# Kernel tuning notes

Hardware: AMD Instinct MI355X
Metric: run time of the kernel (lower is better)

Reference implementation:

```python
import jax, jax.numpy as jnp
import numpy as np

N = 50000
E = 800000
F = 64
HID = 64
HEADS = 4
NTYPES = 3


def layer_norm(x, g, b, eps=1e-5):
    mu = x.mean(-1, keepdims=True)
    var = ((x - mu) ** 2).mean(-1, keepdims=True)
    return (x - mu) * jax.lax.rsqrt(var + eps) * g + b


def gat_conv(x, src, dst, n, W, att_src, att_dst, bias, concat):
    # PyG GATConv: per-head linear transform, additive attention, segment softmax over dst.
    H, C = att_src.shape
    xp = (x @ W).reshape(n, H, C)                       # [N,H,C]
    a_s = (xp * att_src).sum(-1)                         # [N,H]
    a_d = (xp * att_dst).sum(-1)                         # [N,H]
    e = jax.nn.leaky_relu(a_s[src] + a_d[dst], 0.2)      # [Etot,H]
    m = jax.ops.segment_max(e, dst, num_segments=n)      # stable softmax per target
    ex = jnp.exp(e - m[dst])
    denom = jax.ops.segment_sum(ex, dst, num_segments=n)
    alpha = ex / (denom[dst] + 1e-16)                    # [Etot,H]
    msg = xp[src] * alpha[:, :, None]                    # [Etot,H,C]
    out = jax.ops.segment_sum(msg, dst, num_segments=n)  # [N,H,C]
    out = out.reshape(n, H * C) if concat else out.mean(1)
    return out + bias


def setup_inputs() -> dict:
    key = jax.random.key(0)
    ks = jax.random.split(key, 12)
    f32 = jnp.float32
    return {
        'node_features': jax.random.normal(ks[0], (N, F), f32),
        'node_types': jax.random.randint(ks[1], (N,), 0, NTYPES),
        'edge_index': jax.random.randint(ks[2], (2, E), 0, N),
        'type_emb': jax.random.normal(ks[3], (NTYPES, HID), f32) * 0.02,
        'proj_W': jax.random.normal(ks[4], (F, HID), f32) / np.sqrt(F).astype(np.float32),
        'proj_b': jnp.zeros((HID,), f32),
        'W0': jax.random.normal(ks[5], (HID, HEADS * HID), f32) / np.sqrt(HID).astype(np.float32),
        'att_src0': jax.random.normal(ks[6], (HEADS, HID), f32) * 0.1,
        'att_dst0': jax.random.normal(ks[7], (HEADS, HID), f32) * 0.1,
        'bias0': jnp.zeros((HEADS * HID,), f32),
        'ln0_g': jnp.ones((HEADS * HID,), f32),
        'ln0_b': jnp.zeros((HEADS * HID,), f32),
        'W1': jax.random.normal(ks[8], (HEADS * HID, HEADS * HID), f32) / np.sqrt(HEADS * HID).astype(np.float32),
        'att_src1': jax.random.normal(ks[9], (HEADS, HID), f32) * 0.1,
        'att_dst1': jax.random.normal(ks[10], (HEADS, HID), f32) * 0.1,
        'bias1': jnp.zeros((HID,), f32),
        'ln1_g': jnp.ones((HID,), f32),
        'ln1_b': jnp.zeros((HID,), f32),
    }


def reference(node_features, node_types, edge_index, type_emb, proj_W, proj_b,
              W0, att_src0, att_dst0, bias0, ln0_g, ln0_b,
              W1, att_src1, att_dst1, bias1, ln1_g, ln1_b):
    n = node_features.shape[0]
    loop = jnp.arange(n)
    src = jnp.concatenate([edge_index[0], loop])  # add_self_loops=True (PyG default)
    dst = jnp.concatenate([edge_index[1], loop])
    # input projection + node-type embedding
    x = node_features @ proj_W + proj_b + type_emb[node_types]
    # layer 0: concat heads -> [N, HEADS*HID]
    h = gat_conv(x, src, dst, n, W0, att_src0, att_dst0, bias0, True)
    h = jax.nn.relu(layer_norm(h, ln0_g, ln0_b))  # dropout is identity in eval
    # layer 1: mean over heads -> [N, HID]; residual skipped (shape mismatch 256 vs 64)
    h2 = gat_conv(h, src, dst, n, W1, att_src1, att_dst1, bias1, False)
    h2 = jax.nn.relu(layer_norm(h2, ln1_g, ln1_b))
    return h2
```

## Files before the change

### kernel.cpp

```cpp
#include <hip/hip_runtime.h>
#include <hip/hip_bf16.h>
#include <hip/hip_fp16.h>

typedef unsigned short u16;
typedef unsigned int u32;
typedef short s16x8 __attribute__((ext_vector_type(8)));
typedef float f32x4 __attribute__((ext_vector_type(4)));

__device__ __forceinline__ float bf2f(u16 u) {
  return __uint_as_float(((u32)u) << 16);
}

__device__ __forceinline__ u16 f2b(float f) {
  __hip_bfloat16 h = __float2bfloat16(f);
  return *(u16*)&h;
}

__device__ __forceinline__ u32 packbf(float lo, float hi) {
  return (u32)f2b(lo) | ((u32)f2b(hi) << 16);
}

__device__ __forceinline__ bool sniff_bf16(const void* ones) {
  u32 w = *(const u32*)ones;
  return (w >> 16) == (w & 0xFFFFu);
}

__device__ __forceinline__ float ldf(const void* p, size_t i, bool bf) {
  return bf ? bf2f(((const u16*)p)[i]) : ((const float*)p)[i];
}

__device__ __forceinline__ float rdlane_f(float v, int e) {
  return __uint_as_float((u32)__builtin_amdgcn_readlane((int)__float_as_uint(v), e));
}

__global__ void fill_f32(float* __restrict__ p, float v, size_t n) {
  size_t i = (size_t)blockIdx.x * blockDim.x + threadIdx.x;
  if (i < n) p[i] = v;
}

__global__ __launch_bounds__(256) void deg_count_k(const int* __restrict__ ei, int E, int N,
                                                   int* __restrict__ deg) {
  int i = blockIdx.x * 256 + threadIdx.x;
  if (i >= E + N) return;
  int d = (i < E) ? ei[E + i] : (i - E);
  atomicAdd(deg + d, 1);
}

__global__ __launch_bounds__(256) void scan_local_k(const int* __restrict__ deg,
                                                    int* __restrict__ off,
                                                    int* __restrict__ bsum, int N) {
  __shared__ int ps[256];
  int t = threadIdx.x;
  int i = blockIdx.x * 256 + t;
  int v = (i < N) ? deg[i] : 0;
  ps[t] = v;
  __syncthreads();
#pragma unroll
  for (int o = 1; o < 256; o <<= 1) {
    int u = (t >= o) ? ps[t - o] : 0;
    __syncthreads();
    ps[t] += u;
    __syncthreads();
  }
  if (i < N) off[i] = ps[t] - v;
  if (t == 255) bsum[blockIdx.x] = ps[255];
}

__global__ __launch_bounds__(1024) void scan_bsum_k(int* __restrict__ bsum, int nb) {
  __shared__ int ps[1024];
  int t = threadIdx.x;
  int v = (t < nb) ? bsum[t] : 0;
  ps[t] = v;
  __syncthreads();
#pragma unroll
  for (int o = 1; o < 1024; o <<= 1) {
    int u = (t >= o) ? ps[t - o] : 0;
    __syncthreads();
    ps[t] += u;
    __syncthreads();
  }
  if (t < nb) bsum[t] = ps[t] - v;
}

__global__ __launch_bounds__(256) void scan_add_k(int* __restrict__ off,
                                                  const int* __restrict__ bsum,
                                                  int* __restrict__ cur, int N, int Etot) {
  int i = blockIdx.x * 256 + threadIdx.x;
  if (i == 0) off[N] = Etot;
  if (i >= N) return;
  int o = off[i] + bsum[i >> 8];
  off[i] = o;
  cur[i] = o;
}

__global__ __launch_bounds__(256) void scatter_k(const int* __restrict__ ei, int E, int N,
                                                 int* __restrict__ cur, int* __restrict__ csr) {
  int i = blockIdx.x * 256 + threadIdx.x;
  if (i >= E + N) return;
  int s, d;
  if (i < E) { s = ei[i]; d = ei[E + i]; } else { s = i - E; d = s; }
  int p = atomicAdd(cur + d, 1);
  csr[p] = s;
}

__global__ __launch_bounds__(256) void wpack_k(const void* __restrict__ W,
                                               const void* __restrict__ ones,
                                               u16* __restrict__ Wp, int K) {
  bool bf = sniff_bf16(ones);
  int i = blockIdx.x * 256 + threadIdx.x;
  if (i >= K * 256) return;
  int j = i & 7;
  int q = (i >> 3) & 3;
  int c = (i >> 5) & 255;
  int kc = i >> 13;
  int k = kc * 32 + q * 8 + j;
  Wp[i] = f2b(ldf(W, (size_t)k * 256 + c, bf));
}

__global__ __launch_bounds__(256) void wpack64_k(const void* __restrict__ W,
                                                 const void* __restrict__ ones,
                                                 u16* __restrict__ Wp) {
  bool bf = sniff_bf16(ones);
  int i = blockIdx.x * 256 + threadIdx.x;
  if (i >= 64 * 64) return;
  int j = i & 7;
  int q = (i >> 3) & 3;
  int c = (i >> 5) & 63;
  int kc = i >> 11;
  int k = kc * 32 + q * 8 + j;
  Wp[i] = f2b(ldf(W, (size_t)k * 64 + c, bf));
}

__global__ __launch_bounds__(256) void attvec_k(const void* __restrict__ W,
                                                const void* __restrict__ atts,
                                                const void* __restrict__ attd,
                                                const void* __restrict__ ones,
                                                float* __restrict__ va, float* __restrict__ vd) {
  bool bf = sniff_bf16(ones);
  int t = threadIdx.x;
  int h = t >> 6, k = t & 63;
  float s = 0.f, d = 0.f;
  for (int c = 0; c < 64; c++) {
    float w = ldf(W, (size_t)k * 256 + h * 64 + c, bf);
    s += w * ldf(atts, h * 64 + c, bf);
    d += w * ldf(attd, h * 64 + c, bf);
  }
  va[t] = s;
  vd[t] = d;
}

__global__ __launch_bounds__(256) void proj_k(
    const void* __restrict__ nf, const int* __restrict__ ntype,
    const u16* __restrict__ Wpp, const void* __restrict__ pbias,
    const void* __restrict__ temb, const float* __restrict__ va,
    const float* __restrict__ vd, const void* __restrict__ ones,
    u16* __restrict__ x, float* __restrict__ aS, float* __restrict__ aD, int N) {
  bool bf = sniff_bf16(ones);
  __shared__ u16 xs[16][64];
  int t = threadIdx.x;
  int wave = t >> 6, lane = t & 63;
  int r = lane & 15, q = lane >> 4;
  int row0 = blockIdx.x * 16;
  int arow = row0 + r;
  if (arow >= N) arow = N - 1;
  f32x4 xacc = {0.f, 0.f, 0.f, 0.f};
#pragma unroll
  for (int kc = 0; kc < 2; kc++) {
    s16x8 a;
    if (bf) {
      a = *(const s16x8*)((const u16*)nf + (size_t)arow * 64 + kc * 32 + q * 8);
    } else {
      const float* fp = (const float*)nf + (size_t)arow * 64 + kc * 32 + q * 8;
#pragma unroll
      for (int j = 0; j < 8; j++) a[j] = (short)f2b(fp[j]);
    }
    int c = wave * 16 + r;
    s16x8 b = *(const s16x8*)(Wpp + (((size_t)kc * 64 + c) * 4 + q) * 8);
    xacc = __builtin_amdgcn_mfma_f32_16x16x32_bf16(a, b, xacc, 0, 0, 0);
  }
#pragma unroll
  for (int rg = 0; rg < 4; rg++) {
    int row = row0 + q * 4 + rg;
    int rl = (row < N) ? row : N - 1;
    int col = wave * 16 + r;
    int ty = ntype[rl];
    float v = xacc[rg] + ldf(pbias, col, bf) + ldf(temb, ty * 64 + col, bf);
    u16 xb = f2b(v);
    xs[q * 4 + rg][col] = xb;
    if (row < N) x[(size_t)row * 64 + col] = xb;
  }
  __syncthreads();
  float vs[4], vdl[4];
#pragma unroll
  for (int h = 0; h < 4; h++) { vs[h] = va[h * 64 + lane]; vdl[h] = vd[h * 64 + lane]; }
#pragma unroll
  for (int rr = 0; rr < 4; rr++) {
    int row = row0 + wave * 4 + rr;
    float xv = bf2f(xs[wave * 4 + rr][lane]);
    float ps[4], pd[4];
#pragma unroll
    for (int h = 0; h < 4; h++) { ps[h] = xv * vs[h]; pd[h] = xv * vdl[h]; }
#pragma unroll
    for (int o = 32; o > 0; o >>= 1) {
#pragma unroll
      for (int h = 0; h < 4; h++) {
        ps[h] += __shfl_xor(ps[h], o, 64);
        pd[h] += __shfl_xor(pd[h], o, 64);
      }
    }
    if (lane == 0 && row < N) {
#pragma unroll
      for (int h = 0; h < 4; h++) {
        aS[(size_t)row * 4 + h] = ps[h];
        aD[(size_t)row * 4 + h] = pd[h];
      }
    }
  }
}

__global__ __launch_bounds__(256) void agg0_k(
    const int* __restrict__ off, const int* __restrict__ csr,
    const float* __restrict__ aS, const float* __restrict__ aD,
    const u16* __restrict__ x, u16* __restrict__ Ag, int N) {
  int n = blockIdx.x * 4 + (threadIdx.x >> 6);
  int lane = threadIdx.x & 63;
  if (n >= N) return;
  int start = off[n], end = off[n + 1];
  float4 ad4 = *(const float4*)(aD + (size_t)n * 4);
  float ad[4] = {ad4.x, ad4.y, ad4.z, ad4.w};
  float den[4] = {0.f, 0.f, 0.f, 0.f};
  float acc[4] = {0.f, 0.f, 0.f, 0.f};
  const u16* xl = x + lane;

  for (int cs = start; cs < end; cs += 64) {
    int cnt = end - cs; if (cnt > 64) cnt = 64;
    int s = 0;
    float ex[4] = {0.f, 0.f, 0.f, 0.f};
    if (lane < cnt) {
      s = csr[cs + lane];
      float4 as4 = *(const float4*)(aS + (size_t)s * 4);
      float av[4] = {as4.x, as4.y, as4.z, as4.w};
#pragma unroll
      for (int h = 0; h < 4; h++) {
        float v = av[h] + ad[h];
        v = (v > 0.f ? v : 0.2f * v) - 3.0f;
        ex[h] = __expf(v);
        den[h] += ex[h];
      }
    }
#pragma unroll 4
    for (int e = 0; e < cnt; e++) {
      int se = __builtin_amdgcn_readlane(s, e);
      float w0 = rdlane_f(ex[0], e);
      float w1 = rdlane_f(ex[1], e);
      float w2 = rdlane_f(ex[2], e);
      float w3 = rdlane_f(ex[3], e);
      float xv = bf2f(xl[(size_t)se * 64]);
      acc[0] += w0 * xv;
      acc[1] += w1 * xv;
      acc[2] += w2 * xv;
      acc[3] += w3 * xv;
    }
  }
#pragma unroll
  for (int h = 0; h < 4; h++) {
#pragma unroll
    for (int o = 32; o > 0; o >>= 1) den[h] += __shfl_xor(den[h], o, 64);
    acc[h] /= (den[h] + 1e-16f);
  }
#pragma unroll
  for (int h = 0; h < 4; h++) Ag[(size_t)n * 256 + h * 64 + lane] = f2b(acc[h]);
}

__global__ __launch_bounds__(256) void l0post_k(
    const u16* __restrict__ Ag, const u16* __restrict__ Wp,
    const void* __restrict__ bias, const void* __restrict__ g,
    const void* __restrict__ b, const void* __restrict__ ones,
    u16* __restrict__ hb, int N) {
  bool bf = sniff_bf16(ones);
  __shared__ float sm_s[4][16], sm_q[4][16];
  int t = threadIdx.x;
  int wave = t >> 6, lane = t & 63;
  int r = lane & 15, q = lane >> 4;
  int row0 = blockIdx.x * 16;
  int arow = row0 + r;
  if (arow >= N) arow = N - 1;
  const u16* ap = Ag + (size_t)arow * 256 + wave * 64 + q * 8;
  f32x4 acc[4] = {{0.f, 0.f, 0.f, 0.f}, {0.f, 0.f, 0.f, 0.f},
                  {0.f, 0.f, 0.f, 0.f}, {0.f, 0.f, 0.f, 0.f}};
#pragma unroll
  for (int kc = 0; kc < 2; kc++) {
    s16x8 a = *(const s16x8*)(ap + kc * 32);
#pragma unroll
    for (int ct = 0; ct < 4; ct++) {
      int c = wave * 64 + ct * 16 + r;
      s16x8 bb = *(const s16x8*)(Wp + (((size_t)kc * 256 + c) * 4 + q) * 8);
      acc[ct] = __builtin_amdgcn_mfma_f32_16x16x32_bf16(a, bb, acc[ct], 0, 0, 0);
    }
  }
  float yv[4][4];
  float s_p[4] = {0.f, 0.f, 0.f, 0.f};
  float q_p[4] = {0.f, 0.f, 0.f, 0.f};
#pragma unroll
  for (int ct = 0; ct < 4; ct++) {
    float bc = ldf(bias, wave * 64 + ct * 16 + r, bf);
#pragma unroll
    for (int rg = 0; rg < 4; rg++) {
      float y = acc[ct][rg] + bc;
      yv[ct][rg] = y;
      s_p[rg] += y;
      q_p[rg] += y * y;
    }
  }
#pragma unroll
  for (int o = 1; o < 16; o <<= 1) {
#pragma unroll
    for (int rg = 0; rg < 4; rg++) {
      s_p[rg] += __shfl_xor(s_p[rg], o, 64);
      q_p[rg] += __shfl_xor(q_p[rg], o, 64);
    }
  }
  if (r == 0) {
#pragma unroll
    for (int rg = 0; rg < 4; rg++) {
      sm_s[wave][q * 4 + rg] = s_p[rg];
      sm_q[wave][q * 4 + rg] = q_p[rg];
    }
  }
  __syncthreads();
#pragma unroll
  for (int rg = 0; rg < 4; rg++) {
    int lr = q * 4 + rg;
    int row = row0 + lr;
    float mu = (sm_s[0][lr] + sm_s[1][lr] + sm_s[2][lr] + sm_s[3][lr]) * (1.f / 256.f);
    float vq = (sm_q[0][lr] + sm_q[1][lr] + sm_q[2][lr] + sm_q[3][lr]) * (1.f / 256.f) - mu * mu;
    float inv = rsqrtf(vq + 1e-5f);
    if (row < N) {
#pragma unroll
      for (int ct = 0; ct < 4; ct++) {
        int c = wave * 64 + ct * 16 + r;
        float o_ = (yv[ct][rg] - mu) * inv * ldf(g, c, bf) + ldf(b, c, bf);
        hb[(size_t)row * 256 + c] = f2b(fmaxf(o_, 0.f));
      }
    }
  }
}

template <int K>
__global__ __launch_bounds__(256) void gemm_mfma_k(
    const u16* __restrict__ A, const u16* __restrict__ Wp,
    const void* __restrict__ atts, const void* __restrict__ attd,
    const void* __restrict__ ones,
    u16* __restrict__ C, float* __restrict__ aS, float* __restrict__ aD, int N) {
  bool bf = sniff_bf16(ones);
  int t = threadIdx.x;
  int wave = t >> 6, lane = t & 63;
  int r = lane & 15, q = lane >> 4;
  int row0 = blockIdx.x * 16;
  int colw = wave * 64;
  int arow = row0 + r;
  if (arow >= N) arow = N - 1;
  const u16* ap = A + (size_t)arow * K + q * 8;
  f32x4 acc[4] = {{0.f, 0.f, 0.f, 0.f}, {0.f, 0.f, 0.f, 0.f},
                  {0.f, 0.f, 0.f, 0.f}, {0.f, 0.f, 0.f, 0.f}};
#pragma unroll
  for (int kc = 0; kc < K / 32; kc++) {
    s16x8 a = *(const s16x8*)(ap + kc * 32);
#pragma unroll
    for (int ct = 0; ct < 4; ct++) {
      int c = colw + ct * 16 + r;
      s16x8 b = *(const s16x8*)(Wp + (((size_t)kc * 256 + c) * 4 + q) * 8);
      acc[ct] = __builtin_amdgcn_mfma_f32_16x16x32_bf16(a, b, acc[ct], 0, 0, 0);
    }
  }
#pragma unroll
  for (int ct = 0; ct < 4; ct++) {
#pragma unroll
    for (int rg = 0; rg < 4; rg++) {
      int row = row0 + q * 4 + rg;
      if (row < N) C[(size_t)row * 256 + colw + ct * 16 + r] = f2b(acc[ct][rg]);
    }
  }
  float sp[4] = {0.f, 0.f, 0.f, 0.f};
  float dp[4] = {0.f, 0.f, 0.f, 0.f};
#pragma unroll
  for (int ct = 0; ct < 4; ct++) {
    int c = colw + ct * 16 + r;
    float av = ldf(atts, c, bf);
    float dv = ldf(attd, c, bf);
#pragma unroll
    for (int rg = 0; rg < 4; rg++) {
      sp[rg] += acc[ct][rg] * av;
      dp[rg] += acc[ct][rg] * dv;
    }
  }
#pragma unroll
  for (int o = 1; o < 16; o <<= 1) {
#pragma unroll
    for (int rg = 0; rg < 4; rg++) {
      sp[rg] += __shfl_xor(sp[rg], o, 64);
      dp[rg] += __shfl_xor(dp[rg], o, 64);
    }
  }
  if (r == 0) {
#pragma unroll
    for (int rg = 0; rg < 4; rg++) {
      int row = row0 + q * 4 + rg;
      if (row < N) {
        aS[(size_t)row * 4 + wave] = sp[rg];
        aD[(size_t)row * 4 + wave] = dp[rg];
      }
    }
  }
}

__global__ __launch_bounds__(256) void agg1_k(
    const int* __restrict__ off, const int* __restrict__ csr,
    const float* __restrict__ aS, const float* __restrict__ aD,
    const u16* __restrict__ xp,
    const void* __restrict__ bias, const void* __restrict__ g,
    const void* __restrict__ b, void* __restrict__ out, int N) {
  bool bf = sniff_bf16(g);
  int n = blockIdx.x * 4 + (threadIdx.x >> 6);
  int lane = threadIdx.x & 63;
  if (n >= N) return;
  int start = off[n], end = off[n + 1];
  bool hiSel = (lane & 32) != 0;
  float4 ad4 = *(const float4*)(aD + (size_t)n * 4);
  float ad[4] = {ad4.x, ad4.y, ad4.z, ad4.w};
  float den[4] = {0.f, 0.f, 0.f, 0.f};
  float acc[4] = {0.f, 0.f, 0.f, 0.f};
  const u32* xp32 = (const u32*)xp;

  for (int cs = start; cs < end; cs += 64) {
    int cnt = end - cs; if (cnt > 64) cnt = 64;
    int s = 0;
    float ex[4] = {0.f, 0.f, 0.f, 0.f};
    if (lane < cnt) {
      s = csr[cs + lane];
      float4 as4 = *(const float4*)(aS + (size_t)s * 4);
      float av[4] = {as4.x, as4.y, as4.z, as4.w};
#pragma unroll
      for (int h = 0; h < 4; h++) {
        float v = av[h] + ad[h];
        v = (v > 0.f ? v : 0.2f * v) - 3.0f;
        ex[h] = __expf(v);
        den[h] += ex[h];
      }
    }
#pragma unroll 4
    for (int e = 0; e < cnt; e++) {
      int se = __builtin_amdgcn_readlane(s, e);
      float w0 = rdlane_f(ex[0], e);
      float w1 = rdlane_f(ex[1], e);
      float w2 = rdlane_f(ex[2], e);
      float w3 = rdlane_f(ex[3], e);
      float wA = hiSel ? w1 : w0;
      float wB = hiSel ? w3 : w2;
      const u32* xr = xp32 + (size_t)se * 128 + lane;
      u32 dA = xr[0];
      u32 dB = xr[64];
      acc[0] += wA * __uint_as_float(dA << 16);
      acc[1] += wA * __uint_as_float(dA & 0xffff0000u);
      acc[2] += wB * __uint_as_float(dB << 16);
      acc[3] += wB * __uint_as_float(dB & 0xffff0000u);
    }
  }
#pragma unroll
  for (int h = 0; h < 4; h++) {
#pragma unroll
    for (int o = 32; o > 0; o >>= 1) den[h] += __shfl_xor(den[h], o, 64);
  }
  {
    float dA = (hiSel ? den[1] : den[0]) + 1e-16f;
    float dB = (hiSel ? den[3] : den[2]) + 1e-16f;
    acc[0] /= dA; acc[1] /= dA;
    acc[2] /= dB; acc[3] /= dB;
  }
  float p0 = acc[0] + acc[2];
  float p1 = acc[1] + acc[3];
  p0 += __shfl_xor(p0, 32, 64);
  p1 += __shfl_xor(p1, 32, 64);
  int c = 2 * (lane & 31);
  float z0 = 0.25f * p0 + ldf(bias, c, bf);
  float z1 = 0.25f * p1 + ldf(bias, c + 1, bf);
  float sum = z0 + z1;
#pragma unroll
  for (int o = 32; o > 0; o >>= 1) sum += __shfl_xor(sum, o, 64);
  float mu = sum * (1.f / 128.f);
  float d0 = z0 - mu, d1 = z1 - mu;
  float sq = d0 * d0 + d1 * d1;
#pragma unroll
  for (int o = 32; o > 0; o >>= 1) sq += __shfl_xor(sq, o, 64);
  float inv = rsqrtf(sq * (1.f / 128.f) + 1e-5f);
  float y0 = fmaxf(d0 * inv * ldf(g, c, bf) + ldf(b, c, bf), 0.f);
  float y1 = fmaxf(d1 * inv * ldf(g, c + 1, bf) + ldf(b, c + 1, bf), 0.f);
  if (lane < 32) {
    if (bf) {
      ((u32*)out)[(size_t)n * 32 + lane] = packbf(y0, y1);
    } else {
      ((float2*)out)[(size_t)n * 32 + lane] = make_float2(y0, y1);
    }
  }
}

extern "C" void kernel_launch(void* const* d_in, const int* in_sizes, int n_in,
                              void* d_out, int out_size, void* d_ws, size_t ws_size,
                              hipStream_t stream) {
  const void* nf   = d_in[0];
  const int* ntyp  = (const int*)d_in[1];
  const int* ei    = (const int*)d_in[2];
  const void* temb = d_in[3];
  const void* pW   = d_in[4];
  const void* pb   = d_in[5];
  const void* W0   = d_in[6];
  const void* as0  = d_in[7];
  const void* ad0  = d_in[8];
  const void* b0   = d_in[9];
  const void* g0   = d_in[10];
  const void* be0  = d_in[11];
  const void* W1   = d_in[12];
  const void* as1  = d_in[13];
  const void* ad1  = d_in[14];
  const void* b1   = d_in[15];
  const void* g1   = d_in[16];
  const void* be1  = d_in[17];

  int N = in_sizes[0] / 64;
  int E = in_sizes[2] / 2;
  int Etot = E + N;

  u16* Wp0 = (u16*)d_ws;
  u16* Wp1 = Wp0 + 64 * 256;
  u16* Wpp = Wp1 + 256 * 256;
  u16* xb  = Wpp + 64 * 64;
  u16* Ag  = xb + (size_t)N * 64;
  u16* A   = Ag + (size_t)N * 256;
  u16* hb  = A + (size_t)N * 256;
  float* va = (float*)(hb + (size_t)N * 256);
  float* vd = va + 256;
  float* aS = vd + 256;
  float* aD = aS + (size_t)N * 4;
  int* deg  = (int*)(aD + (size_t)N * 4);
  int* off  = deg + N;
  int* csr  = off + N + 1;
  int* bsum = csr + Etot;

  dim3 b256(256);
  int nodeBlocks = (N + 3) / 4;
  int edgeBlocksT = (Etot + 255) / 256;
  int gemmBlocks = (N + 15) / 16;
  int scanBlocks = (N + 255) / 256;

  fill_f32<<<(N + 255) / 256, b256, 0, stream>>>((float*)deg, 0.f, (size_t)N);
  deg_count_k<<<edgeBlocksT, b256, 0, stream>>>(ei, E, N, deg);
  scan_local_k<<<scanBlocks, b256, 0, stream>>>(deg, off, bsum, N);
  scan_bsum_k<<<1, 1024, 0, stream>>>(bsum, scanBlocks);
  scan_add_k<<<scanBlocks, b256, 0, stream>>>(off, bsum, deg, N, Etot);
  scatter_k<<<edgeBlocksT, b256, 0, stream>>>(ei, E, N, deg, csr);
  wpack_k<<<(64 * 256 + 255) / 256, b256, 0, stream>>>(W0, g0, Wp0, 64);
  wpack_k<<<(256 * 256 + 255) / 256, b256, 0, stream>>>(W1, g0, Wp1, 256);
  wpack64_k<<<(64 * 64 + 255) / 256, b256, 0, stream>>>(pW, g0, Wpp);
  attvec_k<<<1, b256, 0, stream>>>(W0, as0, ad0, g0, va, vd);

  proj_k<<<gemmBlocks, b256, 0, stream>>>(nf, ntyp, Wpp, pb, temb, va, vd, g0,
                                          xb, aS, aD, N);
  agg0_k<<<nodeBlocks, b256, 0, stream>>>(off, csr, aS, aD, xb, Ag, N);
  l0post_k<<<gemmBlocks, b256, 0, stream>>>(Ag, Wp0, b0, g0, be0, g0, hb, N);

  gemm_mfma_k<256><<<gemmBlocks, b256, 0, stream>>>(hb, Wp1, as1, ad1, g0, A, aS, aD, N);
  agg1_k<<<nodeBlocks, b256, 0, stream>>>(off, csr, aS, aD, A, b1, g1, be1, d_out, N);
}
```

Measured before the change: 447.7 us.

## Fuse layer-0 post GEMM with layer-1 GEMM and fold attention scores into projection

Merges the layer-0 post-processing kernel (GEMM, bias, LayerNorm, ReLU) with the layer-1 GEMM, so the normalized hidden tile stays in shared memory instead of going out to and back from a global buffer. The attention score vectors are precomputed into a packed weight matrix plus per-type constants, letting the projection kernel produce aS/aD with one extra MFMA instead of a shared-memory pass and shuffle reductions. The aggregation loop unroll is also raised from 4 to 8. This cuts one N×256 round trip and a kernel launch, at the cost of more shared memory per block and some bf16 rounding of the folded attention weights.

```diff
diff --git a/kernel.cpp b/kernel.cpp
--- a/kernel.cpp
+++ b/kernel.cpp
@@ -131,32 +131,60 @@
   Wp[i] = f2b(ldf(W, (size_t)k * 64 + c, bf));
 }
 
-__global__ __launch_bounds__(256) void attvec_k(const void* __restrict__ W,
-                                                const void* __restrict__ atts,
-                                                const void* __restrict__ attd,
-                                                const void* __restrict__ ones,
-                                                float* __restrict__ va, float* __restrict__ vd) {
+__global__ __launch_bounds__(256) void attvec2_k(
+    const void* __restrict__ W0, const void* __restrict__ atts,
+    const void* __restrict__ attd, const void* __restrict__ pW,
+    const void* __restrict__ pb, const void* __restrict__ temb,
+    const void* __restrict__ ones, u16* __restrict__ Wpe, float* __restrict__ ca) {
   bool bf = sniff_bf16(ones);
+  __shared__ float va[256], vd[256];
   int t = threadIdx.x;
   int h = t >> 6, k = t & 63;
-  float s = 0.f, d = 0.f;
-  for (int c = 0; c < 64; c++) {
-    float w = ldf(W, (size_t)k * 256 + h * 64 + c, bf);
-    s += w * ldf(atts, h * 64 + c, bf);
-    d += w * ldf(attd, h * 64 + c, bf);
-  }
-  va[t] = s;
-  vd[t] = d;
-}
-
-__global__ __launch_bounds__(256) void proj_k(
+  {
+    float s = 0.f, d = 0.f;
+    for (int c = 0; c < 64; c++) {
+      float w = ldf(W0, (size_t)k * 256 + h * 64 + c, bf);
+      s += w * ldf(atts, h * 64 + c, bf);
+      d += w * ldf(attd, h * 64 + c, bf);
+    }
+    va[t] = s;
+    vd[t] = d;
+  }
+  __syncthreads();
+  {
+    int i = k;
+    float wa = 0.f, wd = 0.f;
+    for (int kk = 0; kk < 64; kk++) {
+      float wv = ldf(pW, (size_t)i * 64 + kk, bf);
+      wa += wv * va[h * 64 + kk];
+      wd += wv * vd[h * 64 + kk];
+    }
+    int kc = i >> 5, q = (i >> 3) & 3, j = i & 7;
+    Wpe[((kc * 16 + h) * 4 + q) * 8 + j] = f2b(wa);
+    Wpe[((kc * 16 + 4 + h) * 4 + q) * 8 + j] = f2b(wd);
+  }
+  Wpe[256 + t] = 0;
+  Wpe[768 + t] = 0;
+  if (t < 12) {
+    int ty = t >> 2, hh = t & 3;
+    float sa = 0.f, sd = 0.f;
+    for (int kk = 0; kk < 64; kk++) {
+      float bv = ldf(pb, kk, bf) + ldf(temb, ty * 64 + kk, bf);
+      sa += bv * va[hh * 64 + kk];
+      sd += bv * vd[hh * 64 + kk];
+    }
+    ca[t] = sa;
+    ca[12 + t] = sd;
+  }
+}
+
+__global__ __launch_bounds__(256) void proj2_k(
     const void* __restrict__ nf, const int* __restrict__ ntype,
-    const u16* __restrict__ Wpp, const void* __restrict__ pbias,
-    const void* __restrict__ temb, const float* __restrict__ va,
-    const float* __restrict__ vd, const void* __restrict__ ones,
+    const u16* __restrict__ Wpp, const u16* __restrict__ Wpe,
+    const void* __restrict__ pbias, const void* __restrict__ temb,
+    const float* __restrict__ ca, const void* __restrict__ ones,
     u16* __restrict__ x, float* __restrict__ aS, float* __restrict__ aD, int N) {
   bool bf = sniff_bf16(ones);
-  __shared__ u16 xs[16][64];
   int t = threadIdx.x;
   int wave = t >> 6, lane = t & 63;
   int r = lane & 15, q = lane >> 4;
@@ -164,6 +192,7 @@
   int arow = row0 + r;
   if (arow >= N) arow = N - 1;
   f32x4 xacc = {0.f, 0.f, 0.f, 0.f};
+  f32x4 eacc = {0.f, 0.f, 0.f, 0.f};
 #pragma unroll
   for (int kc = 0; kc < 2; kc++) {
     s16x8 a;
@@ -174,46 +203,27 @@
 #pragma unroll
       for (int j = 0; j < 8; j++) a[j] = (short)f2b(fp[j]);
     }
-    int c = wave * 16 + r;
-    s16x8 b = *(const s16x8*)(Wpp + (((size_t)kc * 64 + c) * 4 + q) * 8);
-    xacc = __builtin_amdgcn_mfma_f32_16x16x32_bf16(a, b, xacc, 0, 0, 0);
+    {
+      int c = wave * 16 + r;
+      s16x8 b = *(const s16x8*)(Wpp + (((size_t)kc * 64 + c) * 4 + q) * 8);
+      xacc = __builtin_amdgcn_mfma_f32_16x16x32_bf16(a, b, xacc, 0, 0, 0);
+    }
+    if (wave == 3) {
+      s16x8 b = *(const s16x8*)(Wpe + (((size_t)kc * 16 + r) * 4 + q) * 8);
+      eacc = __builtin_amdgcn_mfma_f32_16x16x32_bf16(a, b, eacc, 0, 0, 0);
+    }
   }
 #pragma unroll
   for (int rg = 0; rg < 4; rg++) {
     int row = row0 + q * 4 + rg;
-    int rl = (row < N) ? row : N - 1;
+    if (row >= N) continue;
     int col = wave * 16 + r;
-    int ty = ntype[rl];
+    int ty = ntype[row];
     float v = xacc[rg] + ldf(pbias, col, bf) + ldf(temb, ty * 64 + col, bf);
-    u16 xb = f2b(v);
-    xs[q * 4 + rg][col] = xb;
-    if (row < N) x[(size_t)row * 64 + col] = xb;
-  }
-  __syncthreads();
-  float vs[4], vdl[4];
-#pragma unroll
-  for (int h = 0; h < 4; h++) { vs[h] = va[h * 64 + lane]; vdl[h] = vd[h * 64 + lane]; }
-#pragma unroll
-  for (int rr = 0; rr < 4; rr++) {
-    int row = row0 + wave * 4 + rr;
-    float xv = bf2f(xs[wave * 4 + rr][lane]);
-    float ps[4], pd[4];
-#pragma unroll
-    for (int h = 0; h < 4; h++) { ps[h] = xv * vs[h]; pd[h] = xv * vdl[h]; }
-#pragma unroll
-    for (int o = 32; o > 0; o >>= 1) {
-#pragma unroll
-      for (int h = 0; h < 4; h++) {
-        ps[h] += __shfl_xor(ps[h], o, 64);
-        pd[h] += __shfl_xor(pd[h], o, 64);
-      }
-    }
-    if (lane == 0 && row < N) {
-#pragma unroll
-      for (int h = 0; h < 4; h++) {
-        aS[(size_t)row * 4 + h] = ps[h];
-        aD[(size_t)row * 4 + h] = pd[h];
-      }
+    x[(size_t)row * 64 + col] = f2b(v);
+    if (wave == 3 && r < 8) {
+      if (r < 4) aS[(size_t)row * 4 + r] = eacc[rg] + ca[ty * 4 + r];
+      else       aD[(size_t)row * 4 + (r - 4)] = eacc[rg] + ca[12 + ty * 4 + (r - 4)];
     }
   }
 }
@@ -248,7 +258,7 @@
         den[h] += ex[h];
       }
     }
-#pragma unroll 4
+#pragma unroll 8
     for (int e = 0; e < cnt; e++) {
       int se = __builtin_amdgcn_readlane(s, e);
       float w0 = rdlane_f(ex[0], e);
@@ -272,12 +282,15 @@
   for (int h = 0; h < 4; h++) Ag[(size_t)n * 256 + h * 64 + lane] = f2b(acc[h]);
 }
 
-__global__ __launch_bounds__(256) void l0post_k(
-    const u16* __restrict__ Ag, const u16* __restrict__ Wp,
-    const void* __restrict__ bias, const void* __restrict__ g,
-    const void* __restrict__ b, const void* __restrict__ ones,
-    u16* __restrict__ hb, int N) {
+__global__ __launch_bounds__(256) void l0g1_k(
+    const u16* __restrict__ Ag, const u16* __restrict__ Wp0,
+    const void* __restrict__ bias0, const void* __restrict__ g0,
+    const void* __restrict__ be0, const u16* __restrict__ Wp1,
+    const void* __restrict__ atts, const void* __restrict__ attd,
+    const void* __restrict__ ones,
+    u16* __restrict__ C, float* __restrict__ aS, float* __restrict__ aD, int N) {
   bool bf = sniff_bf16(ones);
+  __shared__ u16 hs[16][264];
   __shared__ float sm_s[4][16], sm_q[4][16];
   int t = threadIdx.x;
   int wave = t >> 6, lane = t & 63;
@@ -285,91 +298,75 @@
   int row0 = blockIdx.x * 16;
   int arow = row0 + r;
   if (arow >= N) arow = N - 1;
-  const u16* ap = Ag + (size_t)arow * 256 + wave * 64 + q * 8;
+  {
+    const u16* ap = Ag + (size_t)arow * 256 + wave * 64 + q * 8;
+    f32x4 acc[4] = {{0.f, 0.f, 0.f, 0.f}, {0.f, 0.f, 0.f, 0.f},
+                    {0.f, 0.f, 0.f, 0.f}, {0.f, 0.f, 0.f, 0.f}};
+#pragma unroll
+    for (int kc = 0; kc < 2; kc++) {
+      s16x8 a = *(const s16x8*)(ap + kc * 32);
+#pragma unroll
+      for (int ct = 0; ct < 4; ct++) {
+        int c = wave * 64 + ct * 16 + r;
+        s16x8 b = *(const s16x8*)(Wp0 + (((size_t)kc * 256 + c) * 4 + q) * 8);
+        acc[ct] = __builtin_amdgcn_mfma_f32_16x16x32_bf16(a, b, acc[ct], 0, 0, 0);
+      }
+    }
+    float yv[4][4];
+    float s_p[4] = {0.f, 0.f, 0.f, 0.f};
+    float q_p[4] = {0.f, 0.f, 0.f, 0.f};
+#pragma unroll
+    for (int ct = 0; ct < 4; ct++) {
+      float bc = ldf(bias0, wave * 64 + ct * 16 + r, bf);
+#pragma unroll
+      for (int rg = 0; rg < 4; rg++) {
+        float y = acc[ct][rg] + bc;
+        yv[ct][rg] = y;
+        s_p[rg] += y;
+        q_p[rg] += y * y;
+      }
+    }
+#pragma unroll
+    for (int o = 1; o < 16; o <<= 1) {
+#pragma unroll
+      for (int rg = 0; rg < 4; rg++) {
+        s_p[rg] += __shfl_xor(s_p[rg], o, 64);
+        q_p[rg] += __shfl_xor(q_p[rg], o, 64);
+      }
+    }
+    if (r == 0) {
+#pragma unroll
+      for (int rg = 0; rg < 4; rg++) {
+        sm_s[wave][q * 4 + rg] = s_p[rg];
+        sm_q[wave][q * 4 + rg] = q_p[rg];
+      }
+    }
+    __syncthreads();
+#pragma unroll
+    for (int rg = 0; rg < 4; rg++) {
+      int lr = q * 4 + rg;
+      float mu = (sm_s[0][lr] + sm_s[1][lr] + sm_s[2][lr] + sm_s[3][lr]) * (1.f / 256.f);
+      float vq = (sm_q[0][lr] + sm_q[1][lr] + sm_q[2][lr] + sm_q[3][lr]) * (1.f / 256.f) - mu * mu;
+      float inv = rsqrtf(vq + 1e-5f);
+#pragma unroll
+      for (int ct = 0; ct < 4; ct++) {
+        int c = wave * 64 + ct * 16 + r;
+        float o_ = (yv[ct][rg] - mu) * inv * ldf(g0, c, bf) + ldf(be0, c, bf);
+        hs[lr][c] = f2b(fmaxf(o_, 0.f));
+      }
+    }
+  }
+  __syncthreads();
+  int colw = wave * 64;
   f32x4 acc[4] = {{0.f, 0.f, 0.f, 0.f}, {0.f, 0.f, 0.f, 0.f},
                   {0.f, 0.f, 0.f, 0.f}, {0.f, 0.f, 0.f, 0.f}};
 #pragma unroll
-  for (int kc = 0; kc < 2; kc++) {
-    s16x8 a = *(const s16x8*)(ap + kc * 32);
-#pragma unroll
-    for (int ct = 0; ct < 4; ct++) {
-      int c = wave * 64 + ct * 16 + r;
-      s16x8 bb = *(const s16x8*)(Wp + (((size_t)kc * 256 + c) * 4 + q) * 8);
-      acc[ct] = __builtin_amdgcn_mfma_f32_16x16x32_bf16(a, bb, acc[ct], 0, 0, 0);
-    }
-  }
-  float yv[4][4];
-  float s_p[4] = {0.f, 0.f, 0.f, 0.f};
-  float q_p[4] = {0.f, 0.f, 0.f, 0.f};
-#pragma unroll
-  for (int ct = 0; ct < 4; ct++) {
-    float bc = ldf(bias, wave * 64 + ct * 16 + r, bf);
-#pragma unroll
-    for (int rg = 0; rg < 4; rg++) {
-      float y = acc[ct][rg] + bc;
-      yv[ct][rg] = y;
-      s_p[rg] += y;
-      q_p[rg] += y * y;
-    }
-  }
-#pragma unroll
-  for (int o = 1; o < 16; o <<= 1) {
-#pragma unroll
-    for (int rg = 0; rg < 4; rg++) {
-      s_p[rg] += __shfl_xor(s_p[rg], o, 64);
-      q_p[rg] += __shfl_xor(q_p[rg], o, 64);
-    }
-  }
-  if (r == 0) {
-#pragma unroll
-    for (int rg = 0; rg < 4; rg++) {
-      sm_s[wave][q * 4 + rg] = s_p[rg];
-      sm_q[wave][q * 4 + rg] = q_p[rg];
-    }
-  }
-  __syncthreads();
-#pragma unroll
-  for (int rg = 0; rg < 4; rg++) {
-    int lr = q * 4 + rg;
-    int row = row0 + lr;
-    float mu = (sm_s[0][lr] + sm_s[1][lr] + sm_s[2][lr] + sm_s[3][lr]) * (1.f / 256.f);
-    float vq = (sm_q[0][lr] + sm_q[1][lr] + sm_q[2][lr] + sm_q[3][lr]) * (1.f / 256.f) - mu * mu;
-    float inv = rsqrtf(vq + 1e-5f);
-    if (row < N) {
-#pragma unroll
-      for (int ct = 0; ct < 4; ct++) {
-        int c = wave * 64 + ct * 16 + r;
-        float o_ = (yv[ct][rg] - mu) * inv * ldf(g, c, bf) + ldf(b, c, bf);
-        hb[(size_t)row * 256 + c] = f2b(fmaxf(o_, 0.f));
-      }
-    }
-  }
-}
-
-template <int K>
-__global__ __launch_bounds__(256) void gemm_mfma_k(
-    const u16* __restrict__ A, const u16* __restrict__ Wp,
-    const void* __restrict__ atts, const void* __restrict__ attd,
-    const void* __restrict__ ones,
-    u16* __restrict__ C, float* __restrict__ aS, float* __restrict__ aD, int N) {
-  bool bf = sniff_bf16(ones);
-  int t = threadIdx.x;
-  int wave = t >> 6, lane = t & 63;
-  int r = lane & 15, q = lane >> 4;
-  int row0 = blockIdx.x * 16;
-  int colw = wave * 64;
-  int arow = row0 + r;
-  if (arow >= N) arow = N - 1;
-  const u16* ap = A + (size_t)arow * K + q * 8;
-  f32x4 acc[4] = {{0.f, 0.f, 0.f, 0.f}, {0.f, 0.f, 0.f, 0.f},
-                  {0.f, 0.f, 0.f, 0.f}, {0.f, 0.f, 0.f, 0.f}};
-#pragma unroll
-  for (int kc = 0; kc < K / 32; kc++) {
-    s16x8 a = *(const s16x8*)(ap + kc * 32);
+  for (int kc = 0; kc < 8; kc++) {
+    s16x8 a = *(const s16x8*)&hs[r][kc * 32 + q * 8];
 #pragma unroll
     for (int ct = 0; ct < 4; ct++) {
       int c = colw + ct * 16 + r;
-      s16x8 b = *(const s16x8*)(Wp + (((size_t)kc * 256 + c) * 4 + q) * 8);
+      s16x8 b = *(const s16x8*)(Wp1 + (((size_t)kc * 256 + c) * 4 + q) * 8);
       acc[ct] = __builtin_amdgcn_mfma_f32_16x16x32_bf16(a, b, acc[ct], 0, 0, 0);
     }
   }
@@ -448,7 +445,7 @@
         den[h] += ex[h];
       }
     }
-#pragma unroll 4
+#pragma unroll 8
     for (int e = 0; e < cnt; e++) {
       int se = __builtin_amdgcn_readlane(s, e);
       float w0 = rdlane_f(ex[0], e);
@@ -533,15 +530,14 @@
   u16* Wp0 = (u16*)d_ws;
   u16* Wp1 = Wp0 + 64 * 256;
   u16* Wpp = Wp1 + 256 * 256;
-  u16* xb  = Wpp + 64 * 64;
+  u16* Wpe = Wpp + 64 * 64;
+  u16* xb  = Wpe + 1024;
   u16* Ag  = xb + (size_t)N * 64;
   u16* A   = Ag + (size_t)N * 256;
-  u16* hb  = A + (size_t)N * 256;
-  float* va = (float*)(hb + (size_t)N * 256);
-  float* vd = va + 256;
-  float* aS = vd + 256;
+  float* aS = (float*)(A + (size_t)N * 256);
   float* aD = aS + (size_t)N * 4;
-  int* deg  = (int*)(aD + (size_t)N * 4);
+  float* ca = aD + (size_t)N * 4;
+  int* deg  = (int*)(ca + 32);
   int* off  = deg + N;
   int* csr  = off + N + 1;
   int* bsum = csr + Etot;
@@ -561,13 +557,12 @@
   wpack_k<<<(64 * 256 + 255) / 256, b256, 0, stream>>>(W0, g0, Wp0, 64);
   wpack_k<<<(256 * 256 + 255) / 256, b256, 0, stream>>>(W1, g0, Wp1, 256);
   wpack64_k<<<(64 * 64 + 255) / 256, b256, 0, stream>>>(pW, g0, Wpp);
-  attvec_k<<<1, b256, 0, stream>>>(W0, as0, ad0, g0, va, vd);
-
-  proj_k<<<gemmBlocks, b256, 0, stream>>>(nf, ntyp, Wpp, pb, temb, va, vd, g0,
-                                          xb, aS, aD, N);
+  attvec2_k<<<1, b256, 0, stream>>>(W0, as0, ad0, pW, pb, temb, g0, Wpe, ca);
+
+  proj2_k<<<gemmBlocks, b256, 0, stream>>>(nf, ntyp, Wpp, Wpe, pb, temb, ca, g0,
+                                           xb, aS, aD, N);
   agg0_k<<<nodeBlocks, b256, 0, stream>>>(off, csr, aS, aD, xb, Ag, N);
-  l0post_k<<<gemmBlocks, b256, 0, stream>>>(Ag, Wp0, b0, g0, be0, g0, hb, N);
-
-  gemm_mfma_k<256><<<gemmBlocks, b256, 0, stream>>>(hb, Wp1, as1, ad1, g0, A, aS, aD, N);
+  l0g1_k<<<gemmBlocks, b256, 0, stream>>>(Ag, Wp0, b0, g0, be0, Wp1, as1, ad1, g0,
+                                          A, aS, aD, N);
   agg1_k<<<nodeBlocks, b256, 0, stream>>>(off, csr, aS, aD, A, b1, g1, be1, d_out, N);
 }
```

Result: faster. 414.9 us (-7.3%).
